# Optimization experiments

Hardware: AMD Instinct MI355X
Metric: run time of the kernel (lower is better)

## Reference

```python
import jax, jax.numpy as jnp
import numpy as np

N = 80000        # nodes
E = 1280000      # edges
NG = 8           # graphs (segment ids)
F_IN = 3
NC = 20
BN_EPS = 1e-3    # keras BatchNormalization default epsilon


def setup_inputs() -> dict:
    key = jax.random.key(0)
    ks = jax.random.split(key, 16)
    inp = {}
    inp['x'] = jax.random.normal(ks[0], (N, F_IN), dtype=jnp.float32)
    inp['edge_w'] = jax.random.uniform(ks[1], (E,), dtype=jnp.float32)
    inp['src'] = jax.random.randint(ks[2], (E,), 0, N, dtype=jnp.int32)
    inp['dst'] = jax.random.randint(ks[3], (E,), 0, N, dtype=jnp.int32)
    inp['ids'] = jnp.sort(jax.random.randint(ks[4], (N,), 0, NG, dtype=jnp.int32))
    def w(k, fi, fo):
        return jax.random.normal(k, (fi, fo), dtype=jnp.float32) * (1.0 / np.sqrt(fi))
    inp['W1'] = w(ks[5], F_IN, 32); inp['b1'] = jnp.zeros((32,), jnp.float32)
    inp['W2'] = w(ks[6], 32, 32);   inp['b2'] = jnp.zeros((32,), jnp.float32)
    inp['g1'] = jnp.ones((32,), jnp.float32); inp['be1'] = jnp.zeros((32,), jnp.float32)
    inp['m1'] = jax.random.normal(ks[7], (32,), dtype=jnp.float32) * 0.1
    inp['v1'] = jax.random.uniform(ks[8], (32,), dtype=jnp.float32) + 0.5
    inp['W3'] = w(ks[9], 32, 64);   inp['b3'] = jnp.zeros((64,), jnp.float32)
    inp['W4'] = w(ks[10], 64, 64);  inp['b4'] = jnp.zeros((64,), jnp.float32)
    inp['g2'] = jnp.ones((64,), jnp.float32); inp['be2'] = jnp.zeros((64,), jnp.float32)
    inp['m2'] = jax.random.normal(ks[11], (64,), dtype=jnp.float32) * 0.1
    inp['v2'] = jax.random.uniform(ks[12], (64,), dtype=jnp.float32) + 0.5
    inp['W5'] = w(ks[13], 64, NC);  inp['b5'] = jnp.zeros((NC,), jnp.float32)
    return inp


def _gcn(x, W, b, src, dst, ew):
    # Spektral GCNConv: A_norm @ (X W) + b, with A given as edge list (src->dst).
    h = x @ W                                      # [N, Fo] dense transform first (cheaper)
    msg = h[src] * ew[:, None]                     # gather + scale  [E, Fo]
    agg = jax.ops.segment_sum(msg, dst, num_segments=N)  # scatter-add [N, Fo]
    return agg + b


def _bn(x, g, be, m, v):
    # inference-mode BatchNormalization
    return (x - m) * (g * jax.lax.rsqrt(v + BN_EPS)) + be


def _pool(x, ids):
    # per-graph global max pooling, broadcast back to nodes
    mx = jax.ops.segment_max(x, ids, num_segments=NG)   # [NG, F]
    return mx[ids]                                       # [N, F]


def reference(x, edge_w, src, dst, ids,
              W1, b1, W2, b2, g1, be1, m1, v1,
              W3, b3, W4, b4, g2, be2, m2, v2,
              W5, b5):
    h = jax.nn.relu(_gcn(x, W1, b1, src, dst, edge_w))
    h = jax.nn.relu(_gcn(h, W2, b2, src, dst, edge_w))
    h = _bn(h, g1, be1, m1, v1)
    h = _pool(h, ids)
    h = jax.nn.relu(_gcn(h, W3, b3, src, dst, edge_w))
    h = jax.nn.relu(_gcn(h, W4, b4, src, dst, edge_w))
    h = _bn(h, g2, be2, m2, v2)
    h = _pool(h, ids)
    # dropout is identity in inference
    out = jax.nn.softmax(_gcn(h, W5, b5, src, dst, edge_w), axis=-1)
    return out
```

## Files before the change

### kernel.cpp

```cpp
#include <hip/hip_runtime.h>

#define NN 80000
#define NE 1280000
#define NGR 8
#define BN_EPS 1e-3f
#define NB 313
#define GB 320
#define CHK 4000

typedef unsigned short ushort;
typedef __attribute__((ext_vector_type(8))) short bf16x8;
typedef __attribute__((ext_vector_type(4))) float f32x4;

__device__ __forceinline__ unsigned enc_f(float f) {
    unsigned b = __float_as_uint(f);
    return (f >= 0.f) ? (b | 0x80000000u) : ~b;
}
__device__ __forceinline__ float dec_f(unsigned u) {
    return (u & 0x80000000u) ? __uint_as_float(u & 0x7FFFFFFFu) : __uint_as_float(~u);
}
__device__ __forceinline__ ushort f2bf(float f) {
    unsigned u = __float_as_uint(f);
    unsigned r = u + 0x7FFFu + ((u >> 16) & 1u);
    return (ushort)(r >> 16);
}
__device__ __forceinline__ void fma8(float* acc, const ushort* p, float w) {
    uint4 q = *(const uint4*)p;
    acc[0] += w * __uint_as_float((q.x & 0xFFFFu) << 16);
    acc[1] += w * __uint_as_float(q.x & 0xFFFF0000u);
    acc[2] += w * __uint_as_float((q.y & 0xFFFFu) << 16);
    acc[3] += w * __uint_as_float(q.y & 0xFFFF0000u);
    acc[4] += w * __uint_as_float((q.z & 0xFFFFu) << 16);
    acc[5] += w * __uint_as_float(q.z & 0xFFFF0000u);
    acc[6] += w * __uint_as_float((q.w & 0xFFFFu) << 16);
    acc[7] += w * __uint_as_float(q.w & 0xFFFF0000u);
}

__global__ __launch_bounds__(256) void k_bhist(const int* __restrict__ dst,
                                               int* __restrict__ bcnt) {
    __shared__ int lh[NB];
    for (int i = threadIdx.x; i < NB; i += 256) lh[i] = 0;
    __syncthreads();
    int e0 = blockIdx.x * CHK;
    for (int e = e0 + threadIdx.x; e < e0 + CHK; e += 256)
        atomicAdd(&lh[dst[e] >> 8], 1);
    __syncthreads();
    for (int i = threadIdx.x; i < NB; i += 256) {
        int c = lh[i];
        if (c) atomicAdd(&bcnt[i], c);
    }
}

__global__ __launch_bounds__(512) void k_bscan(const int* __restrict__ bcnt,
                                               int* __restrict__ bo,
                                               int* __restrict__ bcur) {
    __shared__ int sm[512];
    int tid = threadIdx.x;
    int v = (tid < NB) ? bcnt[tid] : 0;
    sm[tid] = v;
    __syncthreads();
    #pragma unroll
    for (int off = 1; off < 512; off <<= 1) {
        int t2 = (tid >= off) ? sm[tid - off] : 0;
        __syncthreads();
        sm[tid] += t2;
        __syncthreads();
    }
    if (tid < NB) {
        int ex = sm[tid] - v;
        bo[tid] = ex;
        bcur[tid] = ex;
    }
    if (tid == 0) bo[NB] = NE;
}

__global__ __launch_bounds__(256) void k_bfill(const int* __restrict__ src,
                                               const int* __restrict__ dst,
                                               const float* __restrict__ ew,
                                               const int* __restrict__ ids,
                                               int* __restrict__ bcur,
                                               int2* __restrict__ cB) {
    __shared__ int lh[NB];
    __shared__ int lbase[NB];
    for (int i = threadIdx.x; i < NB; i += 256) lh[i] = 0;
    __syncthreads();
    int e0 = blockIdx.x * CHK;
    for (int e = e0 + threadIdx.x; e < e0 + CHK; e += 256)
        atomicAdd(&lh[dst[e] >> 8], 1);
    __syncthreads();
    for (int i = threadIdx.x; i < NB; i += 256) {
        int c = lh[i];
        lbase[i] = c ? atomicAdd(&bcur[i], c) : 0;
        lh[i] = 0;
    }
    __syncthreads();
    for (int e = e0 + threadIdx.x; e < e0 + CHK; e += 256) {
        int d = dst[e];
        int b = d >> 8;
        int s = src[e];
        int pos = lbase[b] + atomicAdd(&lh[b], 1);
        cB[pos] = make_int2(s | (ids[s] << 17) | ((d & 255) << 20),
                            __float_as_int(ew[e]));
    }
}

__global__ __launch_bounds__(256) void k_insort(const int* __restrict__ bo,
                                                const int2* __restrict__ cB,
                                                int* __restrict__ rp,
                                                int2* __restrict__ cE) {
    __shared__ int lc[256];
    __shared__ int loff[256];
    __shared__ int sm[256];
    int b = blockIdx.x, tid = threadIdx.x;
    int s0 = bo[b], s1 = bo[b + 1];
    lc[tid] = 0;
    __syncthreads();
    for (int i = s0 + tid; i < s1; i += 256)
        atomicAdd(&lc[(cB[i].x >> 20) & 255], 1);
    __syncthreads();
    int v = lc[tid];
    sm[tid] = v;
    __syncthreads();
    #pragma unroll
    for (int off = 1; off < 256; off <<= 1) {
        int t2 = (tid >= off) ? sm[tid - off] : 0;
        __syncthreads();
        sm[tid] += t2;
        __syncthreads();
    }
    loff[tid] = sm[tid] - v;
    int n = b * 256 + tid;
    if (n < NN) rp[n] = s0 + loff[tid];
    if (b == NB - 1 && tid == 0) rp[NN] = NE;
    lc[tid] = 0;
    __syncthreads();
    for (int i = s0 + tid; i < s1; i += 256) {
        int2 a = cB[i];
        int dlow = (a.x >> 20) & 255;
        int pos = s0 + loff[dlow] + atomicAdd(&lc[dlow], 1);
        cE[pos] = make_int2((a.x & 0x1FFFF) | (((a.x >> 17) & 7) << 24), a.y);
    }
}

__global__ __launch_bounds__(256) void k_wprep(const float* __restrict__ W2,
                                               const float* __restrict__ W4,
                                               ushort* __restrict__ W2t,
                                               ushort* __restrict__ W4t) {
    int t = threadIdx.x;
    for (int i = t; i < 32 * 32; i += 256) {
        int f = i >> 5, k = i & 31;
        W2t[i] = f2bf(W2[k * 32 + f]);
    }
    for (int i = t; i < 64 * 64; i += 256) {
        int f = i >> 6, k = i & 63;
        W4t[i] = f2bf(W4[k * 64 + f]);
    }
}

__global__ __launch_bounds__(256) void k_gSX(const float* __restrict__ x,
                                             const int* __restrict__ rp,
                                             const int2* __restrict__ cE,
                                             float* __restrict__ S,
                                             float* __restrict__ AX) {
    int n = blockIdx.x * 256 + threadIdx.x;
    if (n >= NN) return;
    int e0 = rp[n], e1 = rp[n + 1];
    float sv[8] = {0, 0, 0, 0, 0, 0, 0, 0};
    float ax0 = 0.f, ax1 = 0.f, ax2 = 0.f;
    for (int i = e0; i < e1; ++i) {
        int2 a = cE[i];
        float w = __int_as_float(a.y);
        int s = a.x & 0xFFFFFF;
        int gg = a.x >> 24;
        #pragma unroll
        for (int g = 0; g < 8; ++g) sv[g] += (gg == g) ? w : 0.f;
        const float* xp = x + s * 3;
        ax0 += w * xp[0]; ax1 += w * xp[1]; ax2 += w * xp[2];
    }
    float4* Sp = (float4*)(S + n * 8);
    Sp[0] = make_float4(sv[0], sv[1], sv[2], sv[3]);
    Sp[1] = make_float4(sv[4], sv[5], sv[6], sv[7]);
    *(float4*)(AX + n * 4) = make_float4(ax0, ax1, ax2, 0.f);
}

__global__ __launch_bounds__(256) void k_l12m(const float* __restrict__ AX,
                                              const float* __restrict__ W1,
                                              const float* __restrict__ b1,
                                              const ushort* __restrict__ W2t,
                                              ushort* __restrict__ T) {
    __shared__ ushort h1s[64 * 40];
    int t = threadIdx.x;
    int nb = blockIdx.x * 64;
    {
        int f = t & 31, rr = t >> 5;
        float w0 = W1[f], w1 = W1[32 + f], w2 = W1[64 + f], bb = b1[f];
        #pragma unroll
        for (int i = 0; i < 8; ++i) {
            int n = rr + i * 8;
            float4 ax = *(const float4*)(AX + (nb + n) * 4);
            float acc = bb + ax.x * w0 + ax.y * w1 + ax.z * w2;
            h1s[n * 40 + f] = f2bf(fmaxf(acc, 0.f));
        }
    }
    __syncthreads();
    int lane = t & 63, wave = t >> 6;
    int quad = lane >> 4, col = lane & 15;
    int mtile = wave;
    bf16x8 a = *(const bf16x8*)(h1s + (mtile * 16 + col) * 40 + quad * 8);
    #pragma unroll
    for (int ntile = 0; ntile < 2; ++ntile) {
        bf16x8 b = *(const bf16x8*)(W2t + (ntile * 16 + col) * 32 + quad * 8);
        f32x4 acc = {0.f, 0.f, 0.f, 0.f};
        acc = __builtin_amdgcn_mfma_f32_16x16x32_bf16(a, b, acc, 0, 0, 0);
        #pragma unroll
        for (int r = 0; r < 4; ++r) {
            int node = nb + mtile * 16 + quad * 4 + r;
            T[node * 32 + ntile * 16 + col] = f2bf(acc[r]);
        }
    }
}

__global__ __launch_bounds__(256) void k_l34m(const float* __restrict__ S,
                                              const float* __restrict__ HW3,
                                              const float* __restrict__ b3,
                                              const ushort* __restrict__ W4t,
                                              ushort* __restrict__ T) {
    __shared__ ushort h3s[64 * 72];
    int t = threadIdx.x;
    int nb = blockIdx.x * 64;
    {
        int f = t & 63, rr = t >> 6;
        float hwc[8];
        #pragma unroll
        for (int g = 0; g < 8; ++g) hwc[g] = HW3[g * 64 + f];
        float bb = b3[f];
        #pragma unroll
        for (int i = 0; i < 16; ++i) {
            int n = rr + i * 4;
            const float4* sp = (const float4*)(S + (size_t)(nb + n) * 8);
            float4 s0 = sp[0], s1 = sp[1];
            float acc = bb + s0.x * hwc[0] + s0.y * hwc[1] + s0.z * hwc[2] +
                        s0.w * hwc[3] + s1.x * hwc[4] + s1.y * hwc[5] +
                        s1.z * hwc[6] + s1.w * hwc[7];
            h3s[n * 72 + f] = f2bf(fmaxf(acc, 0.f));
        }
    }
    __syncthreads();
    int lane = t & 63, wave = t >> 6;
    int quad = lane >> 4, col = lane & 15;
    int mtile = wave;
    bf16x8 a0 = *(const bf16x8*)(h3s + (mtile * 16 + col) * 72 + quad * 8);
    bf16x8 a1 = *(const bf16x8*)(h3s + (mtile * 16 + col) * 72 + 32 + quad * 8);
    #pragma unroll
    for (int ntile = 0; ntile < 4; ++ntile) {
        bf16x8 b0 = *(const bf16x8*)(W4t + (ntile * 16 + col) * 64 + quad * 8);
        bf16x8 b1v = *(const bf16x8*)(W4t + (ntile * 16 + col) * 64 + 32 + quad * 8);
        f32x4 acc = {0.f, 0.f, 0.f, 0.f};
        acc = __builtin_amdgcn_mfma_f32_16x16x32_bf16(a0, b0, acc, 0, 0, 0);
        acc = __builtin_amdgcn_mfma_f32_16x16x32_bf16(a1, b1v, acc, 0, 0, 0);
        #pragma unroll
        for (int r = 0; r < 4; ++r) {
            int node = nb + mtile * 16 + quad * 4 + r;
            T[node * 64 + ntile * 16 + col] = f2bf(acc[r]);
        }
    }
}

template <int LOGF>
__global__ __launch_bounds__(256) void k_gpool(const ushort* __restrict__ th,
                                               const int* __restrict__ rp,
                                               const int2* __restrict__ cE,
                                               const int* __restrict__ ids,
                                               const float* __restrict__ b,
                                               const float* __restrict__ g,
                                               const float* __restrict__ be,
                                               const float* __restrict__ m,
                                               const float* __restrict__ v,
                                               unsigned* __restrict__ mxe) {
    const int F = 1 << LOGF;
    const int CPN = F >> 3;
    const int NPB = 256 / CPN;
    __shared__ unsigned lmx[NGR * F];
    for (int i = threadIdx.x; i < NGR * F; i += 256) lmx[i] = 0u;
    __syncthreads();
    int c = threadIdx.x & (CPN - 1);
    int n = blockIdx.x * NPB + (threadIdx.x >> (LOGF - 3));
    if (n < NN) {
        int e0 = rp[n], e1 = rp[n + 1];
        float acc[8] = {0, 0, 0, 0, 0, 0, 0, 0};
        float acc2[8] = {0, 0, 0, 0, 0, 0, 0, 0};
        int i = e0;
        for (; i + 2 <= e1; i += 2) {
            int2 a0 = cE[i], a1 = cE[i + 1];
            const ushort* p0 = th + (((size_t)(a0.x & 0xFFFFFF)) << LOGF) + (c << 3);
            const ushort* p1 = th + (((size_t)(a1.x & 0xFFFFFF)) << LOGF) + (c << 3);
            fma8(acc, p0, __int_as_float(a0.y));
            fma8(acc2, p1, __int_as_float(a1.y));
        }
        if (i < e1) {
            int2 a0 = cE[i];
            fma8(acc, th + (((size_t)(a0.x & 0xFFFFFF)) << LOGF) + (c << 3),
                 __int_as_float(a0.y));
        }
        int gg = ids[n];
        #pragma unroll
        for (int j = 0; j < 8; ++j) {
            int f = (c << 3) + j;
            float scale = g[f] * rsqrtf(v[f] + BN_EPS);
            float h = fmaxf(acc[j] + acc2[j] + b[f], 0.f);
            float val = (h - m[f]) * scale + be[f];
            atomicMax(&lmx[gg * F + f], enc_f(val));
        }
    }
    __syncthreads();
    for (int i = threadIdx.x; i < NGR * F; i += 256) {
        unsigned u = lmx[i];
        if (u) atomicMax(&mxe[i], u);
    }
}

__global__ __launch_bounds__(512) void k_dechw3(const unsigned* __restrict__ mxe,
                                                const float* __restrict__ W,
                                                float* __restrict__ HW) {
    __shared__ float smx[256];
    int t = threadIdx.x;
    if (t < 256) smx[t] = mxe[t] ? dec_f(mxe[t]) : 0.f;
    __syncthreads();
    int g = t >> 6, f = t & 63;
    float acc = 0.f;
    #pragma unroll
    for (int k = 0; k < 32; ++k) acc += smx[g * 32 + k] * W[k * 64 + f];
    HW[t] = acc;
}

__global__ __launch_bounds__(512) void k_dechw5(const unsigned* __restrict__ mxe,
                                                const float* __restrict__ W,
                                                float* __restrict__ HW) {
    __shared__ float smx[512];
    int t = threadIdx.x;
    smx[t] = mxe[t] ? dec_f(mxe[t]) : 0.f;
    __syncthreads();
    if (t >= 160) return;
    int g = t / 20, c = t % 20;
    float acc = 0.f;
    #pragma unroll
    for (int k = 0; k < 64; ++k) acc += smx[g * 64 + k] * W[k * 20 + c];
    HW[t] = acc;
}

__global__ __launch_bounds__(256) void k_out(const float* __restrict__ S,
                                             const float* __restrict__ HW5,
                                             const float* __restrict__ b5,
                                             float* __restrict__ out) {
    __shared__ float hw[160];
    __shared__ float bb[20];
    int t = threadIdx.x;
    if (t < 160) hw[t] = HW5[t];
    if (t < 20) bb[t] = b5[t];
    __syncthreads();
    int n = blockIdx.x * 256 + t;
    if (n >= NN) return;
    const float4* sp = (const float4*)(S + n * 8);
    float4 s0 = sp[0], s1 = sp[1];
    float sv[8] = {s0.x, s0.y, s0.z, s0.w, s1.x, s1.y, s1.z, s1.w};
    float pre[20];
    #pragma unroll
    for (int c = 0; c < 20; ++c) {
        float acc = bb[c];
        #pragma unroll
        for (int g = 0; g < 8; ++g) acc += sv[g] * hw[g * 20 + c];
        pre[c] = acc;
    }
    float mx = pre[0];
    #pragma unroll
    for (int c = 1; c < 20; ++c) mx = fmaxf(mx, pre[c]);
    float sum = 0.f;
    #pragma unroll
    for (int c = 0; c < 20; ++c) { pre[c] = __expf(pre[c] - mx); sum += pre[c]; }
    float inv = 1.f / sum;
    #pragma unroll
    for (int c = 0; c < 20; ++c) out[n * 20 + c] = pre[c] * inv;
}

extern "C" void kernel_launch(void* const* d_in, const int* in_sizes, int n_in,
                              void* d_out, int out_size, void* d_ws, size_t ws_size,
                              hipStream_t stream) {
    const float* x   = (const float*)d_in[0];
    const float* ew  = (const float*)d_in[1];
    const int*   src = (const int*)d_in[2];
    const int*   dst = (const int*)d_in[3];
    const int*   ids = (const int*)d_in[4];
    const float* W1 = (const float*)d_in[5];  const float* b1 = (const float*)d_in[6];
    const float* W2 = (const float*)d_in[7];  const float* b2 = (const float*)d_in[8];
    const float* g1 = (const float*)d_in[9];  const float* be1 = (const float*)d_in[10];
    const float* m1 = (const float*)d_in[11]; const float* v1 = (const float*)d_in[12];
    const float* W3 = (const float*)d_in[13]; const float* b3 = (const float*)d_in[14];
    const float* W4 = (const float*)d_in[15]; const float* b4 = (const float*)d_in[16];
    const float* g2 = (const float*)d_in[17]; const float* be2 = (const float*)d_in[18];
    const float* m2 = (const float*)d_in[19]; const float* v2 = (const float*)d_in[20];
    const float* W5 = (const float*)d_in[21]; const float* b5 = (const float*)d_in[22];
    float* out = (float*)d_out;

    char* p = (char*)d_ws;
    float*  S    = (float*)p;  p += (size_t)NN * 8 * 4;
    ushort* T    = (ushort*)p; p += (size_t)NN * 64 * 2;
    float*  AX   = (float*)p;  p += (size_t)NN * 4 * 4;
    int*    rp   = (int*)p;    p += (size_t)(NN + 16) * 4;
    int*    bcnt = (int*)p;    p += 512 * 4;
    int*    bo   = (int*)p;    p += 512 * 4;
    int*    bcur = (int*)p;    p += 512 * 4;
    int2*   cB   = (int2*)p;   p += (size_t)NE * 8;
    int2*   cE   = (int2*)p;   p += (size_t)NE * 8;
    unsigned* MXE1 = (unsigned*)p; p += 256 * 4;
    unsigned* MXE2 = (unsigned*)p; p += 512 * 4;
    float*  HW3  = (float*)p;  p += 512 * 4;
    float*  HW5  = (float*)p;  p += 256 * 4;
    ushort* W2t  = (ushort*)p; p += 1024 * 2;
    ushort* W4t  = (ushort*)p; p += 4096 * 2;

    const int BS = 256;
    const int gN = (NN + BS - 1) / BS;

    hipMemsetAsync(bcnt, 0, 512 * 4, stream);
    hipMemsetAsync(MXE1, 0, 768 * 4, stream);
    hipLaunchKernelGGL(k_wprep, dim3(1), dim3(BS), 0, stream, W2, W4, W2t, W4t);
    hipLaunchKernelGGL(k_bhist, dim3(GB), dim3(BS), 0, stream, dst, bcnt);
    hipLaunchKernelGGL(k_bscan, dim3(1), dim3(512), 0, stream, bcnt, bo, bcur);
    hipLaunchKernelGGL(k_bfill, dim3(GB), dim3(BS), 0, stream, src, dst, ew, ids, bcur, cB);
    hipLaunchKernelGGL(k_insort, dim3(NB), dim3(BS), 0, stream, bo, cB, rp, cE);

    hipLaunchKernelGGL(k_gSX, dim3(gN), dim3(BS), 0, stream, x, rp, cE, S, AX);

    hipLaunchKernelGGL(k_l12m, dim3(NN / 64), dim3(BS), 0, stream, AX, W1, b1, W2t, T);
    hipLaunchKernelGGL(k_gpool<5>, dim3(NN / 64), dim3(BS), 0, stream, T, rp, cE, ids, b2, g1, be1, m1, v1, MXE1);

    hipLaunchKernelGGL(k_dechw3, dim3(1), dim3(512), 0, stream, MXE1, W3, HW3);
    hipLaunchKernelGGL(k_l34m, dim3(NN / 64), dim3(BS), 0, stream, S, HW3, b3, W4t, T);
    hipLaunchKernelGGL(k_gpool<6>, dim3(NN / 32), dim3(BS), 0, stream, T, rp, cE, ids, b4, g2, be2, m2, v2, MXE2);

    hipLaunchKernelGGL(k_dechw5, dim3(1), dim3(512), 0, stream, MXE2, W5, HW5);
    hipLaunchKernelGGL(k_out, dim3(gN), dim3(BS), 0, stream, S, HW5, b5, out);
}
```

Baseline: 276.0 us.

## Replace atomic bucket offsets with per-block histogram scan in CSR build

The counting sort used to build CSR by destination is restructured. Each block now writes its own 625-bin histogram (128 nodes per bin). A per-bin column scan plus a global scan then gives every block deterministic base offsets, so bfill no longer re-histograms or takes global atomics. Bins are smaller and there are more chunks, which raises parallelism in bfill and insort. The cost is extra histogram traffic (1280x625 ints) and one more kernel launch.

Result: no change. 274.1 us (-0.7%).

```diff
diff --git a/kernel.cpp b/kernel.cpp
--- a/kernel.cpp
+++ b/kernel.cpp
@@ -4,9 +4,9 @@
 #define NE 1280000
 #define NGR 8
 #define BN_EPS 1e-3f
-#define NB 313
-#define GB 320
-#define CHK 4000
+#define NBF 625
+#define GB 1280
+#define CHK 1000
 
 typedef unsigned short ushort;
 typedef __attribute__((ext_vector_type(8))) short bf16x8;
@@ -37,106 +37,120 @@
 }
 
 __global__ __launch_bounds__(256) void k_bhist(const int* __restrict__ dst,
-                                               int* __restrict__ bcnt) {
-    __shared__ int lh[NB];
-    for (int i = threadIdx.x; i < NB; i += 256) lh[i] = 0;
+                                               int* __restrict__ hcnt) {
+    __shared__ int lh[NBF];
+    for (int i = threadIdx.x; i < NBF; i += 256) lh[i] = 0;
     __syncthreads();
     int e0 = blockIdx.x * CHK;
     for (int e = e0 + threadIdx.x; e < e0 + CHK; e += 256)
-        atomicAdd(&lh[dst[e] >> 8], 1);
-    __syncthreads();
-    for (int i = threadIdx.x; i < NB; i += 256) {
-        int c = lh[i];
-        if (c) atomicAdd(&bcnt[i], c);
-    }
-}
-
-__global__ __launch_bounds__(512) void k_bscan(const int* __restrict__ bcnt,
-                                               int* __restrict__ bo,
-                                               int* __restrict__ bcur) {
-    __shared__ int sm[512];
-    int tid = threadIdx.x;
-    int v = (tid < NB) ? bcnt[tid] : 0;
-    sm[tid] = v;
-    __syncthreads();
-    #pragma unroll
-    for (int off = 1; off < 512; off <<= 1) {
-        int t2 = (tid >= off) ? sm[tid - off] : 0;
-        __syncthreads();
-        sm[tid] += t2;
-        __syncthreads();
-    }
-    if (tid < NB) {
-        int ex = sm[tid] - v;
-        bo[tid] = ex;
-        bcur[tid] = ex;
-    }
-    if (tid == 0) bo[NB] = NE;
+        atomicAdd(&lh[dst[e] >> 7], 1);
+    __syncthreads();
+    int* row = hcnt + (size_t)blockIdx.x * NBF;
+    for (int i = threadIdx.x; i < NBF; i += 256) row[i] = lh[i];
+}
+
+__global__ __launch_bounds__(256) void k_bbase1(int* __restrict__ hcnt,
+                                                int* __restrict__ tot) {
+    __shared__ int sm[256];
+    int bin = blockIdx.x, t = threadIdx.x;
+    int v[5];
+    int s = 0;
+    #pragma unroll
+    for (int j = 0; j < 5; ++j) {
+        v[j] = hcnt[(size_t)(t * 5 + j) * NBF + bin];
+        s += v[j];
+    }
+    sm[t] = s;
+    __syncthreads();
+    #pragma unroll
+    for (int off = 1; off < 256; off <<= 1) {
+        int u = (t >= off) ? sm[t - off] : 0;
+        __syncthreads();
+        sm[t] += u;
+        __syncthreads();
+    }
+    int run = sm[t] - s;
+    if (t == 255) tot[bin] = sm[255];
+    #pragma unroll
+    for (int j = 0; j < 5; ++j) {
+        hcnt[(size_t)(t * 5 + j) * NBF + bin] = run;
+        run += v[j];
+    }
+}
+
+__global__ __launch_bounds__(1024) void k_bbase2(const int* __restrict__ tot,
+                                                 int* __restrict__ bo) {
+    __shared__ int sm[1024];
+    int t = threadIdx.x;
+    int v = (t < NBF) ? tot[t] : 0;
+    sm[t] = v;
+    __syncthreads();
+    #pragma unroll
+    for (int off = 1; off < 1024; off <<= 1) {
+        int u = (t >= off) ? sm[t - off] : 0;
+        __syncthreads();
+        sm[t] += u;
+        __syncthreads();
+    }
+    if (t < NBF) bo[t] = sm[t] - v;
+    if (t == 0) bo[NBF] = NE;
 }
 
 __global__ __launch_bounds__(256) void k_bfill(const int* __restrict__ src,
                                                const int* __restrict__ dst,
                                                const float* __restrict__ ew,
                                                const int* __restrict__ ids,
-                                               int* __restrict__ bcur,
+                                               const int* __restrict__ hcnt,
+                                               const int* __restrict__ bo,
                                                int2* __restrict__ cB) {
-    __shared__ int lh[NB];
-    __shared__ int lbase[NB];
-    for (int i = threadIdx.x; i < NB; i += 256) lh[i] = 0;
+    __shared__ int lcur[NBF];
+    const int* row = hcnt + (size_t)blockIdx.x * NBF;
+    for (int i = threadIdx.x; i < NBF; i += 256) lcur[i] = row[i] + bo[i];
     __syncthreads();
     int e0 = blockIdx.x * CHK;
-    for (int e = e0 + threadIdx.x; e < e0 + CHK; e += 256)
-        atomicAdd(&lh[dst[e] >> 8], 1);
-    __syncthreads();
-    for (int i = threadIdx.x; i < NB; i += 256) {
-        int c = lh[i];
-        lbase[i] = c ? atomicAdd(&bcur[i], c) : 0;
-        lh[i] = 0;
-    }
-    __syncthreads();
     for (int e = e0 + threadIdx.x; e < e0 + CHK; e += 256) {
         int d = dst[e];
-        int b = d >> 8;
         int s = src[e];
-        int pos = lbase[b] + atomicAdd(&lh[b], 1);
-        cB[pos] = make_int2(s | (ids[s] << 17) | ((d & 255) << 20),
+        int pos = atomicAdd(&lcur[d >> 7], 1);
+        cB[pos] = make_int2(s | (ids[s] << 17) | ((d & 127) << 20),
                             __float_as_int(ew[e]));
     }
 }
 
-__global__ __launch_bounds__(256) void k_insort(const int* __restrict__ bo,
+__global__ __launch_bounds__(512) void k_insort(const int* __restrict__ bo,
                                                 const int2* __restrict__ cB,
                                                 int* __restrict__ rp,
                                                 int2* __restrict__ cE) {
-    __shared__ int lc[256];
-    __shared__ int loff[256];
-    __shared__ int sm[256];
-    int b = blockIdx.x, tid = threadIdx.x;
-    int s0 = bo[b], s1 = bo[b + 1];
-    lc[tid] = 0;
-    __syncthreads();
-    for (int i = s0 + tid; i < s1; i += 256)
-        atomicAdd(&lc[(cB[i].x >> 20) & 255], 1);
-    __syncthreads();
-    int v = lc[tid];
-    sm[tid] = v;
-    __syncthreads();
-    #pragma unroll
-    for (int off = 1; off < 256; off <<= 1) {
-        int t2 = (tid >= off) ? sm[tid - off] : 0;
-        __syncthreads();
-        sm[tid] += t2;
-        __syncthreads();
-    }
-    loff[tid] = sm[tid] - v;
-    int n = b * 256 + tid;
-    if (n < NN) rp[n] = s0 + loff[tid];
-    if (b == NB - 1 && tid == 0) rp[NN] = NE;
-    lc[tid] = 0;
-    __syncthreads();
-    for (int i = s0 + tid; i < s1; i += 256) {
+    __shared__ int lc[128];
+    __shared__ int loff[128];
+    __shared__ int sm[512];
+    int bin = blockIdx.x, t = threadIdx.x;
+    int s0 = bo[bin], s1 = bo[bin + 1];
+    if (t < 128) lc[t] = 0;
+    __syncthreads();
+    for (int i = s0 + t; i < s1; i += 512)
+        atomicAdd(&lc[(cB[i].x >> 20) & 127], 1);
+    __syncthreads();
+    int v = (t < 128) ? lc[t] : 0;
+    sm[t] = v;
+    __syncthreads();
+    #pragma unroll
+    for (int off = 1; off < 128; off <<= 1) {
+        int u = (t >= off && t < 128) ? sm[t - off] : 0;
+        __syncthreads();
+        if (t < 128) sm[t] += u;
+        __syncthreads();
+    }
+    if (t < 128) {
+        loff[t] = sm[t] - v;
+        rp[bin * 128 + t] = s0 + loff[t];
+        lc[t] = 0;
+    }
+    if (bin == NBF - 1 && t == 0) rp[NN] = NE;
+    __syncthreads();
+    for (int i = s0 + t; i < s1; i += 512) {
         int2 a = cB[i];
-        int dlow = (a.x >> 20) & 255;
+        int dlow = (a.x >> 20) & 127;
         int pos = s0 + loff[dlow] + atomicAdd(&lc[dlow], 1);
         cE[pos] = make_int2((a.x & 0x1FFFF) | (((a.x >> 17) & 7) << 24), a.y);
     }
@@ -406,9 +420,9 @@
     ushort* T    = (ushort*)p; p += (size_t)NN * 64 * 2;
     float*  AX   = (float*)p;  p += (size_t)NN * 4 * 4;
     int*    rp   = (int*)p;    p += (size_t)(NN + 16) * 4;
-    int*    bcnt = (int*)p;    p += 512 * 4;
-    int*    bo   = (int*)p;    p += 512 * 4;
-    int*    bcur = (int*)p;    p += 512 * 4;
+    int*    hcnt = (int*)p;    p += (size_t)GB * NBF * 4;
+    int*    tot  = (int*)p;    p += 1024 * 4;
+    int*    bo   = (int*)p;    p += 1024 * 4;
     int2*   cB   = (int2*)p;   p += (size_t)NE * 8;
     int2*   cE   = (int2*)p;   p += (size_t)NE * 8;
     unsigned* MXE1 = (unsigned*)p; p += 256 * 4;
@@ -421,13 +435,13 @@
     const int BS = 256;
     const int gN = (NN + BS - 1) / BS;
 
-    hipMemsetAsync(bcnt, 0, 512 * 4, stream);
     hipMemsetAsync(MXE1, 0, 768 * 4, stream);
     hipLaunchKernelGGL(k_wprep, dim3(1), dim3(BS), 0, stream, W2, W4, W2t, W4t);
-    hipLaunchKernelGGL(k_bhist, dim3(GB), dim3(BS), 0, stream, dst, bcnt);
-    hipLaunchKernelGGL(k_bscan, dim3(1), dim3(512), 0, stream, bcnt, bo, bcur);
-    hipLaunchKernelGGL(k_bfill, dim3(GB), dim3(BS), 0, stream, src, dst, ew, ids, bcur, cB);
-    hipLaunchKernelGGL(k_insort, dim3(NB), dim3(BS), 0, stream, bo, cB, rp, cE);
+    hipLaunchKernelGGL(k_bhist, dim3(GB), dim3(BS), 0, stream, dst, hcnt);
+    hipLaunchKernelGGL(k_bbase1, dim3(NBF), dim3(BS), 0, stream, hcnt, tot);
+    hipLaunchKernelGGL(k_bbase2, dim3(1), dim3(1024), 0, stream, tot, bo);
+    hipLaunchKernelGGL(k_bfill, dim3(GB), dim3(BS), 0, stream, src, dst, ew, ids, hcnt, bo, cB);
+    hipLaunchKernelGGL(k_insort, dim3(NBF), dim3(512), 0, stream, bo, cB, rp, cE);
 
     hipLaunchKernelGGL(k_gSX, dim3(gN), dim3(BS), 0, stream, x, rp, cE, S, AX);
 
```
